# Kernel tuning notes

Measured on AMD Instinct MI355X. Metric: run time of the kernel, lower is better.

## Reference

```python
import jax, jax.numpy as jnp
import numpy as np

VOCAB = 50000
EMB = 300      # embedding_dim
VDIM = 16      # value_dim
QDIM = 200     # query_dim
NHEAD = 16     # head_num
HIDDEN = VDIM * NHEAD  # 256


def setup_inputs() -> dict:
    key = jax.random.key(0)
    ks = jax.random.split(key, 9)
    news_batch = jax.random.randint(ks[0], (32, 50, 20), 0, VOCAB)  # [B, his, L]
    emb_table = jax.random.normal(ks[1], (VOCAB, EMB), dtype=jnp.float32)
    queryWeight = jax.random.normal(ks[2], (NHEAD, EMB, EMB), dtype=jnp.float32) * 0.05
    queryBias = jax.random.normal(ks[3], (NHEAD, 1, EMB), dtype=jnp.float32) * 0.05
    valueWeight = jax.random.normal(ks[4], (NHEAD, EMB, VDIM), dtype=jnp.float32) * 0.05
    valueBias = jax.random.normal(ks[5], (NHEAD, 1, VDIM), dtype=jnp.float32) * 0.05
    keyW = jax.random.normal(ks[6], (QDIM, HIDDEN), dtype=jnp.float32) * 0.05  # nn.Linear weight [out,in]
    keyB = jax.random.normal(ks[7], (QDIM,), dtype=jnp.float32) * 0.05
    query = jax.random.normal(ks[8], (1, QDIM), dtype=jnp.float32)
    return {"news_batch": news_batch, "emb_table": emb_table,
            "queryWeight": queryWeight, "queryBias": queryBias,
            "valueWeight": valueWeight, "valueBias": valueBias,
            "keyW": keyW, "keyB": keyB, "query": query}


def reference(news_batch, emb_table, queryWeight, queryBias, valueWeight, valueBias, keyW, keyB, query):
    # Dropout in eval mode -> identity.
    x = emb_table[news_batch]                                   # [B,S,L,E]
    B, S, L, E = x.shape
    # per-head query projection: mha_key.matmul(queryWeight) + queryBias
    q = jnp.einsum('bsle,nef->bsnlf', x, queryWeight) + queryBias  # [B,S,N,L,E]
    # ScaledDpAttention(q, key=x, value=x), scale by sqrt(query last dim) = sqrt(E)
    scores = jnp.einsum('bsnlf,bsmf->bsnlm', q, x) / jnp.sqrt(jnp.float32(E))
    attn = jax.nn.softmax(scores, axis=-1)
    ctx = jnp.einsum('bsnlm,bsme->bsnle', attn, x)               # [B,S,N,L,E]
    v = jnp.einsum('bsnle,nev->bsnlv', ctx, valueWeight) + valueBias  # [B,S,N,L,V]
    # transpose(-2,-3) then merge heads -> [B,S,L,N*V]
    mha_embedding = jnp.swapaxes(v, -2, -3).reshape(B, S, L, HIDDEN)
    # additive attention pooling
    add_key = jnp.tanh(mha_embedding @ keyW.T + keyB)            # [B,S,L,QDIM]
    s2 = jnp.einsum('qd,bsld->bsql', query, add_key) / jnp.sqrt(jnp.float32(QDIM))
    a2 = jax.nn.softmax(s2, axis=-1)                             # [B,S,1,L]
    news_repr = jnp.einsum('bsql,bslh->bsqh', a2, mha_embedding)[:, :, 0, :]  # [B,S,H]
    news_embedding = mha_embedding.reshape(B, S, L, 1, HIDDEN)   # level=1
    return news_embedding, news_repr
```

## Files before the change

kernel.cpp:

```cpp
#include <hip/hip_runtime.h>
#include <math.h>

#define NBS 1600
#define LL 20
#define EE 300
#define NH 16
#define VD 16
#define HID 256
#define QD 200

typedef short bf16x8 __attribute__((ext_vector_type(8)));
typedef float f32x4 __attribute__((ext_vector_type(4)));

__device__ __forceinline__ short f2b(float f) {
    union { float f; unsigned u; } c; c.f = f;
    unsigned r = (c.u + 0x7FFFu + ((c.u >> 16) & 1u)) >> 16;
    return (short)r;
}

__device__ __forceinline__ float b2f(short s) {
    union { unsigned u; float f; } c; c.u = ((unsigned)(unsigned short)s) << 16;
    return c.f;
}

__device__ __forceinline__ float ftanh(float a) {
    a = fminf(fmaxf(a, -15.f), 15.f);
    float t = __expf(2.f * a);
    return (t - 1.f) / (t + 1.f);
}

__device__ __forceinline__ void gload16(const short* g, short* l) {
    __builtin_amdgcn_global_load_lds(
        (const __attribute__((address_space(1))) unsigned int*)g,
        (__attribute__((address_space(3))) unsigned int*)l, 16, 0, 0);
}


__global__ void build_xb_lin(const int* __restrict__ news, const float* __restrict__ emb,
                             short* __restrict__ Xb) {
    int idx = blockIdx.x * 256 + threadIdx.x;
    if (idx >= 32000 * 80) return;
    int i = idx / 80, e4 = (idx % 80) * 4;
    short4 o;
    if (e4 < 300) {
        const float4 v = *reinterpret_cast<const float4*>(emb + (size_t)news[i] * EE + e4);
        o.x = f2b(v.x); o.y = f2b(v.y); o.z = f2b(v.z); o.w = f2b(v.w);
    } else if (e4 == 300) {
        o.x = (short)0x3F80; o.y = 0; o.z = 0; o.w = 0;
    } else {
        o.x = o.y = o.z = o.w = 0;
    }
    *reinterpret_cast<short4*>(Xb + (size_t)i * 320 + e4) = o;
}

__global__ __launch_bounds__(1024) void build_wqt_lin(
    const float* __restrict__ qW, const float* __restrict__ qB, short* __restrict__ WqT)
{
    __shared__ float t[32][33];
    const int n = blockIdx.z;
    const int e0 = blockIdx.x * 32, f0 = blockIdx.y * 32;
    const int tx = threadIdx.x, ty = threadIdx.y;
    const int e = e0 + ty, f = f0 + tx;
    t[ty][tx] = (e < EE && f < EE) ? qW[((size_t)n * EE + e) * EE + f] : 0.f;
    __syncthreads();
    const int fo = f0 + ty, eo = e0 + tx;
    float val;
    if (fo >= EE)      val = 0.f;
    else if (eo < EE)  val = t[tx][ty];
    else if (eo == EE) val = qB[n * EE + fo];
    else               val = 0.f;
    WqT[((size_t)n * 320 + fo) * 320 + eo] = f2b(val);
}

__global__ void build_wvt(const float* __restrict__ vW, const float* __restrict__ vB,
                          short* __restrict__ WvT) {
    int idx = blockIdx.x * 256 + threadIdx.x;
    if (idx >= 256 * 320) return;
    int c = idx / 320, e = idx % 320;
    int n = c >> 4, vd = c & 15;
    float val = (e < EE) ? vW[((size_t)n * EE + e) * VD + vd]
                         : (e == EE ? vB[n * VD + vd] : 0.f);
    WvT[idx] = f2b(val);
}

__global__ void conv_kw(const float* __restrict__ keyW, short* __restrict__ kwb) {
    int idx = blockIdx.x * 256 + threadIdx.x;
    if (idx >= 256 * 256) return;
    int d = idx >> 8;
    kwb[idx] = (d < QD) ? f2b(keyW[idx]) : (short)0;
}

__global__ __launch_bounds__(256) void gemm_xv(
    const short* __restrict__ Xb, const short* __restrict__ WvT, short* __restrict__ xv)
{
    const int nt0 = blockIdx.x * 128;
    const size_t mt0 = (size_t)blockIdx.y * 128;
    const int tid = threadIdx.x, wave = tid >> 6, lane = tid & 63;
    const int lr = lane & 15, lg = lane >> 4;
    const int wm = wave & 1, wn = wave >> 1;

    __shared__ short As[128][68];
    __shared__ short Bs[128][68];
    f32x4 acc[4][4] = {};

    for (int ks = 0; ks < 5; ++ks) {
        __syncthreads();
        for (int u = 0; u < 4; ++u) {
            int idx = u * 256 + tid;
            int rr = idx >> 3, c8 = idx & 7;
            *reinterpret_cast<bf16x8*>(&As[rr][c8 * 8]) =
                *reinterpret_cast<const bf16x8*>(Xb + (mt0 + rr) * 320 + ks * 64 + c8 * 8);
            *reinterpret_cast<bf16x8*>(&Bs[rr][c8 * 8]) =
                *reinterpret_cast<const bf16x8*>(WvT + (size_t)(nt0 + rr) * 320 + ks * 64 + c8 * 8);
        }
        __syncthreads();
        #pragma unroll
        for (int kk = 0; kk < 2; ++kk) {
            bf16x8 af[4], bfv[4];
            #pragma unroll
            for (int f = 0; f < 4; ++f)
                af[f] = *reinterpret_cast<const bf16x8*>(&As[wm * 64 + f * 16 + lr][kk * 32 + lg * 8]);
            #pragma unroll
            for (int f = 0; f < 4; ++f)
                bfv[f] = *reinterpret_cast<const bf16x8*>(&Bs[wn * 64 + f * 16 + lr][kk * 32 + lg * 8]);
            #pragma unroll
            for (int i = 0; i < 4; ++i)
                #pragma unroll
                for (int j = 0; j < 4; ++j)
                    acc[i][j] = __builtin_amdgcn_mfma_f32_16x16x32_bf16(af[i], bfv[j], acc[i][j], 0, 0, 0);
        }
    }
    #pragma unroll
    for (int i = 0; i < 4; ++i)
        #pragma unroll
        for (int j = 0; j < 4; ++j)
            #pragma unroll
            for (int r = 0; r < 4; ++r)
                xv[(mt0 + wm * 64 + i * 16 + lg * 4 + r) * 256 + nt0 + wn * 64 + j * 16 + lr]
                    = f2b(acc[i][j][r]);
}

__global__ __launch_bounds__(256, 2) void qsv(
    const short* __restrict__ Xb,
    const short* __restrict__ WqT,
    const short* __restrict__ xv,
    float*       __restrict__ out1,
    short*       __restrict__ mhb)
{
    const int g = blockIdx.x;
    const int n = blockIdx.y;
    const int tid = threadIdx.x, wave = tid >> 6, lane = tid & 63;
    const int lr = lane & 15, lg = lane >> 4;
    const size_t row0 = (size_t)g * 80;

    __shared__ short lds[25920];

    const short* gp[13];
    #pragma unroll
    for (int k = 0; k < 13; ++k) {
        const int s = k * 256 + tid;
        if (s < 640) {
            const int row = s >> 3, p = s & 7;
            gp[k] = Xb + (row0 + row) * 320 + (p ^ (row & 7)) * 8;
        } else if (s < 3200) {
            const int s2 = s - 640;
            const int row = s2 >> 3, p = s2 & 7;
            gp[k] = WqT + (size_t)(n * 320 + row) * 320 + (p ^ (row & 7)) * 8;
        } else {
            gp[k] = Xb;
        }
    }

    const int b = wave;
    bf16x8 bv;
    #pragma unroll
    for (int j = 0; j < 8; ++j) {
        int m = lg * 8 + j; if (m > 19) m = 19;
        bv[j] = xv[(row0 + b * 20 + m) * 256 + n * 16 + lr];
    }

    const int sw = (lr & 7);

    f32x4 acc[5][5] = {};
    for (int ks = 0; ks < 5; ++ks) {
        __syncthreads();
        const int ko = ks * 64;
        #pragma unroll
        for (int k = 0; k < 12; ++k)
            gload16(gp[k] + ko, lds + (size_t)(k * 256 + tid) * 8);
        if (tid < 128)
            gload16(gp[12] + ko, lds + (size_t)(3072 + tid) * 8);
        __syncthreads();
        #pragma unroll
        for (int sub = 0; sub < 2; ++sub) {
            bf16x8 af[5], bfr[5];
            #pragma unroll
            for (int i = 0; i < 5; ++i)
                af[i] = *reinterpret_cast<const bf16x8*>(
                    lds + (i * 16 + lr) * 64 + ((sub * 4 + lg) ^ sw) * 8);
            #pragma unroll
            for (int j = 0; j < 5; ++j)
                bfr[j] = *reinterpret_cast<const bf16x8*>(
                    lds + 5120 + (wave * 80 + j * 16 + lr) * 64 + ((sub * 4 + lg) ^ sw) * 8);
            #pragma unroll
            for (int i = 0; i < 5; ++i)
                #pragma unroll
                for (int j = 0; j < 5; ++j)
                    acc[i][j] = __builtin_amdgcn_mfma_f32_16x16x32_bf16(af[i], bfr[j], acc[i][j], 0, 0, 0);
        }
    }
    __syncthreads();

    #pragma unroll
    for (int i = 0; i < 5; ++i)
        #pragma unroll
        for (int j = 0; j < 5; ++j)
            #pragma unroll
            for (int r = 0; r < 4; ++r)
                lds[(i * 16 + lg * 4 + r) * 324 + wave * 80 + j * 16 + lr] = f2b(acc[i][j][r]);

    const int rA0 = b * 20 + lr;
    int rA1 = b * 20 + 16 + lr; if (rA1 > 79) rA1 = 79;
    bf16x8 xpre0[10], xpre1[10];
    #pragma unroll
    for (int ks = 0; ks < 10; ++ks) {
        xpre0[ks] = *reinterpret_cast<const bf16x8*>(Xb + (row0 + rA0) * 320 + ks * 32 + lg * 8);
        xpre1[ks] = *reinterpret_cast<const bf16x8*>(Xb + (row0 + rA1) * 320 + ks * 32 + lg * 8);
    }
    __syncthreads();

    float w0[2][4], w1[2][4];
    {
        f32x4 s[2][2] = {};
        #pragma unroll
        for (int ks = 0; ks < 10; ++ks) {
            const int kc = ks * 32 + lg * 8;
            bf16x8 a0 = *reinterpret_cast<const bf16x8*>(lds + rA0 * 324 + kc);
            bf16x8 a1 = *reinterpret_cast<const bf16x8*>(lds + rA1 * 324 + kc);
            s[0][0] = __builtin_amdgcn_mfma_f32_16x16x32_bf16(a0, xpre0[ks], s[0][0], 0, 0, 0);
            s[0][1] = __builtin_amdgcn_mfma_f32_16x16x32_bf16(a0, xpre1[ks], s[0][1], 0, 0, 0);
            s[1][0] = __builtin_amdgcn_mfma_f32_16x16x32_bf16(a1, xpre0[ks], s[1][0], 0, 0, 0);
            s[1][1] = __builtin_amdgcn_mfma_f32_16x16x32_bf16(a1, xpre1[ks], s[1][1], 0, 0, 0);
        }

        const float scl = 0.057735026918962584f;
        #pragma unroll
        for (int mts = 0; mts < 2; ++mts) {
            #pragma unroll
            for (int r = 0; r < 4; ++r) {
                float v0 = s[mts][0][r] * scl;
                float v1 = s[mts][1][r] * scl;
                float mx = (lr < 4) ? fmaxf(v0, v1) : v0;
                mx = fmaxf(mx, __shfl_xor(mx, 1));
                mx = fmaxf(mx, __shfl_xor(mx, 2));
                mx = fmaxf(mx, __shfl_xor(mx, 4));
                mx = fmaxf(mx, __shfl_xor(mx, 8));
                float e0 = __expf(v0 - mx);
                float e1 = (lr < 4) ? __expf(v1 - mx) : 0.f;
                float sm = e0 + e1;
                sm += __shfl_xor(sm, 1);
                sm += __shfl_xor(sm, 2);
                sm += __shfl_xor(sm, 4);
                sm += __shfl_xor(sm, 8);
                const float inv = 1.f / sm;
                w0[mts][r] = e0 * inv;
                w1[mts][r] = e1 * inv;
            }
        }
    }

    short* atw = lds + b * 6480;
    {
        int* az = reinterpret_cast<int*>(atw);
        #pragma unroll
        for (int i = 0; i < 9; ++i) {
            const int ix = lane + i * 64;
            if (ix < 544) az[ix] = 0;
        }
    }
    #pragma unroll
    for (int mts = 0; mts < 2; ++mts)
        #pragma unroll
        for (int r = 0; r < 4; ++r) {
            const int row = mts * 16 + lg * 4 + r;
            if (row < LL) {
                atw[row * 34 + lr]      = f2b(w0[mts][r]);
                atw[row * 34 + 16 + lr] = f2b(w1[mts][r]);
            }
        }

    bf16x8 va0 = *reinterpret_cast<const bf16x8*>(atw + lr * 34 + lg * 8);
    bf16x8 va1 = *reinterpret_cast<const bf16x8*>(atw + (16 + lr) * 34 + lg * 8);
    f32x4 z = {0.f, 0.f, 0.f, 0.f};
    f32x4 v0 = __builtin_amdgcn_mfma_f32_16x16x32_bf16(va0, bv, z, 0, 0, 0);
    f32x4 v1 = __builtin_amdgcn_mfma_f32_16x16x32_bf16(va1, bv, z, 0, 0, 0);
    #pragma unroll
    for (int r = 0; r < 4; ++r) {
        const int rowl = lg * 4 + r;
        const size_t o0 = (row0 + b * 20 + rowl) * 256 + n * 16 + lr;
        out1[o0] = v0[r];
        mhb[o0] = f2b(v0[r]);
        const int rowl1 = 16 + lg * 4 + r;
        if (rowl1 < LL) {
            const size_t o1 = (row0 + b * 20 + rowl1) * 256 + n * 16 + lr;
            out1[o1] = v1[r];
            mhb[o1] = f2b(v1[r]);
        }
    }
}

__global__ __launch_bounds__(256, 4) void gemm_ak(
    const short* __restrict__ mhb,
    const short* __restrict__ kwb,
    short*       __restrict__ ak)
{
    const int nt0 = blockIdx.x * 128;
    const int mt0 = blockIdx.y * 128;
    const int tid = threadIdx.x, wave = tid >> 6, lane = tid & 63;
    const int lr = lane & 15, lg = lane >> 4;
    const int wm = wave & 1, wn = wave >> 1;

    __shared__ short sAB[8192];

    const int rA = tid >> 2, c = tid & 3;
    const short* aS0 = mhb + (size_t)(mt0 + rA) * 256 + c * 8;
    const short* aS1 = aS0 + (size_t)64 * 256;
    const short* bS0 = kwb + (size_t)(nt0 + rA) * 256 + c * 8;
    const short* bS1 = bS0 + (size_t)64 * 256;
    short* d0 = sAB + tid * 8;
    short* d1 = sAB + (tid + 256) * 8;
    short* d2 = sAB + (tid + 512) * 8;
    short* d3 = sAB + (tid + 768) * 8;

    f32x4 acc[4][4] = {};
    for (int ks = 0; ks < 8; ++ks) {
        __syncthreads();
        const int ko = ks * 32;
        gload16(aS0 + ko, d0);
        gload16(aS1 + ko, d1);
        gload16(bS0 + ko, d2);
        gload16(bS1 + ko, d3);
        __syncthreads();
        bf16x8 af[4], bfr[4];
        #pragma unroll
        for (int i = 0; i < 4; ++i)
            af[i] = *reinterpret_cast<const bf16x8*>(sAB + (wm * 64 + i * 16 + lr) * 32 + lg * 8);
        #pragma unroll
        for (int j = 0; j < 4; ++j)
            bfr[j] = *reinterpret_cast<const bf16x8*>(sAB + 4096 + (wn * 64 + j * 16 + lr) * 32 + lg * 8);
        #pragma unroll
        for (int i = 0; i < 4; ++i)
            #pragma unroll
            for (int j = 0; j < 4; ++j)
                acc[i][j] = __builtin_amdgcn_mfma_f32_16x16x32_bf16(af[i], bfr[j], acc[i][j], 0, 0, 0);
    }

    #pragma unroll
    for (int i = 0; i < 4; ++i)
        #pragma unroll
        for (int j = 0; j < 4; ++j)
            #pragma unroll
            for (int r = 0; r < 4; ++r)
                ak[(size_t)(mt0 + wm * 64 + i * 16 + lg * 4 + r) * 256
                   + nt0 + wn * 64 + j * 16 + lr] = f2b(acc[i][j][r]);
}

__global__ __launch_bounds__(256) void pool_light(
    const short* __restrict__ ak,
    const float* __restrict__ out1,
    const float* __restrict__ keyB,
    const float* __restrict__ query,
    float*       __restrict__ out2)
{
    const int bs = blockIdx.x;
    const int tid = threadIdx.x, wave = tid >> 6, lane = tid & 63;

    __shared__ float s2[LL];

    #pragma unroll
    for (int li = 0; li < 5; ++li) {
        const int l = wave * 5 + li;
        const short* ar = ak + ((size_t)bs * 20 + l) * 256;
        float acc = 0.f;
        #pragma unroll
        for (int it = 0; it < 4; ++it) {
            const int d = lane + it * 64;
            if (d < QD) {
                const float t = ftanh(b2f(ar[d]) + keyB[d]);
                acc = fmaf(query[d], t, acc);
            }
        }
        acc += __shfl_xor(acc, 32);
        acc += __shfl_xor(acc, 16);
        acc += __shfl_xor(acc, 8);
        acc += __shfl_xor(acc, 4);
        acc += __shfl_xor(acc, 2);
        acc += __shfl_xor(acc, 1);
        if (lane == 0) s2[l] = acc * 0.07071067811865475f;
    }
    __syncthreads();

    if (tid == 0) {
        float mx = -1e30f;
        #pragma unroll
        for (int l = 0; l < LL; ++l) mx = fmaxf(mx, s2[l]);
        float e[LL], sum = 0.f;
        #pragma unroll
        for (int l = 0; l < LL; ++l) { e[l] = __expf(s2[l] - mx); sum += e[l]; }
        const float inv = 1.f / sum;
        #pragma unroll
        for (int l = 0; l < LL; ++l) s2[l] = e[l] * inv;
    }
    __syncthreads();

    float o = 0.f;
    #pragma unroll
    for (int l = 0; l < LL; ++l)
        o = fmaf(s2[l], out1[((size_t)bs * 20 + l) * 256 + tid], o);
    out2[(size_t)bs * 256 + tid] = o;
}


#define XP 330
#define TP 42
#define AP 34

__global__ __launch_bounds__(1024) void transpose_qw(
    const float* __restrict__ qW, short* __restrict__ wqt)
{
    __shared__ float t[32][33];
    const int n = blockIdx.z;
    const int e0 = blockIdx.x * 32, f0 = blockIdx.y * 32;
    const int tx = threadIdx.x, ty = threadIdx.y;
    const int e = e0 + ty, f = f0 + tx;
    t[ty][tx] = (e < EE && f < EE) ? qW[(size_t)n * EE * EE + e * EE + f] : 0.f;
    __syncthreads();
    const int fo = f0 + ty, eo = e0 + tx;
    if (fo < 304)
        wqt[(size_t)n * 304 * 320 + fo * 320 + eo] = f2b(t[tx][ty]);
}

__global__ void conv_vw(const float* __restrict__ vW, short* __restrict__ wvt) {
    int idx = blockIdx.x * 256 + threadIdx.x;
    if (idx >= NH * VD * 320) return;
    int e = idx % 320;
    int v = (idx / 320) % VD;
    int n = idx / (320 * VD);
    wvt[idx] = (e < EE) ? f2b(vW[(size_t)n * EE * VD + e * VD + v]) : (short)0;
}

__global__ __launch_bounds__(512) void nrms_attn_mfma(
    const int*   __restrict__ news,
    const float* __restrict__ emb,
    const short* __restrict__ wqt,
    const float* __restrict__ qB,
    const short* __restrict__ wvt,
    const float* __restrict__ vB,
    float*       __restrict__ out1)
{
    const int bs   = blockIdx.x;
    const int tid  = threadIdx.x;
    const int wave = tid >> 6;
    const int lane = tid & 63;
    const int lr   = lane & 15;
    const int lg   = lane >> 4;

    __shared__ short xs[32][XP];
    __shared__ short xT[320][TP];
    __shared__ short qs[32][XP];
    __shared__ float sc[32][33];
    __shared__ short at[32][AP];

    {
        int* z = (int*)&xs[0][0];
        for (int i = tid; i < 32 * XP / 2; i += 512) z[i] = 0;
        z = (int*)&qs[0][0];
        for (int i = tid; i < 32 * XP / 2; i += 512) z[i] = 0;
        z = (int*)&xT[0][0];
        for (int i = tid; i < 320 * TP / 2; i += 512) z[i] = 0;
    }
    __syncthreads();

    for (int idx = tid; idx < LL * 75; idx += 512) {
        const int l = idx / 75, e4 = (idx % 75) * 4;
        const int row = news[bs * LL + l];
        const float4 v = *reinterpret_cast<const float4*>(emb + (size_t)row * EE + e4);
        const short b0 = f2b(v.x), b1 = f2b(v.y), b2 = f2b(v.z), b3 = f2b(v.w);
        xs[l][e4] = b0; xs[l][e4 + 1] = b1; xs[l][e4 + 2] = b2; xs[l][e4 + 3] = b3;
        xT[e4][l] = b0; xT[e4 + 1][l] = b1; xT[e4 + 2][l] = b2; xT[e4 + 3][l] = b3;
    }
    __syncthreads();

    for (int n = 0; n < NH; ++n) {
        const short* wq = wqt + (size_t)n * 304 * 320;

        for (int p = wave; p < 19; p += 8) {
            f32x4 acc0 = {0.f, 0.f, 0.f, 0.f};
            f32x4 acc1 = {0.f, 0.f, 0.f, 0.f};
            const short* a0p = &xs[lr][lg * 8];
            const short* a1p = &xs[16 + lr][lg * 8];
            const short* bp  = wq + (p * 16 + lr) * 320 + lg * 8;
            #pragma unroll
            for (int k = 0; k < 10; ++k) {
                bf16x8 b  = *reinterpret_cast<const bf16x8*>(bp + k * 32);
                bf16x8 a0 = *reinterpret_cast<const bf16x8*>(a0p + k * 32);
                bf16x8 a1 = *reinterpret_cast<const bf16x8*>(a1p + k * 32);
                acc0 = __builtin_amdgcn_mfma_f32_16x16x32_bf16(a0, b, acc0, 0, 0, 0);
                acc1 = __builtin_amdgcn_mfma_f32_16x16x32_bf16(a1, b, acc1, 0, 0, 0);
            }
            const int col = p * 16 + lr;
            const float bias = (col < EE) ? qB[n * EE + col] : 0.f;
            #pragma unroll
            for (int r = 0; r < 4; ++r) {
                qs[lg * 4 + r][col]      = f2b(acc0[r] + bias);
                qs[16 + lg * 4 + r][col] = f2b(acc1[r] + bias);
            }
        }
        __syncthreads();

        if (wave < 4) {
            const int mt = wave & 1, nt = wave >> 1;
            f32x4 acc = {0.f, 0.f, 0.f, 0.f};
            const short* ap = &qs[mt * 16 + lr][lg * 8];
            const short* bp = &xs[nt * 16 + lr][lg * 8];
            #pragma unroll
            for (int k = 0; k < 10; ++k) {
                bf16x8 a = *reinterpret_cast<const bf16x8*>(ap + k * 32);
                bf16x8 b = *reinterpret_cast<const bf16x8*>(bp + k * 32);
                acc = __builtin_amdgcn_mfma_f32_16x16x32_bf16(a, b, acc, 0, 0, 0);
            }
            #pragma unroll
            for (int r = 0; r < 4; ++r)
                sc[mt * 16 + lg * 4 + r][nt * 16 + lr] = acc[r] * 0.057735026918962584f;
        }
        __syncthreads();

        if (tid < LL) {
            float mx = -1e30f;
            #pragma unroll
            for (int m = 0; m < LL; ++m) mx = fmaxf(mx, sc[tid][m]);
            float ev[LL], sum = 0.f;
            #pragma unroll
            for (int m = 0; m < LL; ++m) { ev[m] = __expf(sc[tid][m] - mx); sum += ev[m]; }
            const float inv = 1.f / sum;
            #pragma unroll
            for (int m = 0; m < LL; ++m) at[tid][m] = f2b(ev[m] * inv);
            #pragma unroll
            for (int m = LL; m < 32; ++m) at[tid][m] = 0;
        } else if (tid < 32) {
            int* zr = (int*)&at[tid][0];
            #pragma unroll
            for (int m = 0; m < 16; ++m) zr[m] = 0;
        }
        __syncthreads();

        for (int p = wave; p < 19; p += 8) {
            bf16x8 b  = *reinterpret_cast<const bf16x8*>(&xT[p * 16 + lr][lg * 8]);
            bf16x8 a0 = *reinterpret_cast<const bf16x8*>(&at[lr][lg * 8]);
            bf16x8 a1 = *reinterpret_cast<const bf16x8*>(&at[16 + lr][lg * 8]);
            f32x4 z = {0.f, 0.f, 0.f, 0.f};
            f32x4 c0 = __builtin_amdgcn_mfma_f32_16x16x32_bf16(a0, b, z, 0, 0, 0);
            f32x4 c1 = __builtin_amdgcn_mfma_f32_16x16x32_bf16(a1, b, z, 0, 0, 0);
            const int col = p * 16 + lr;
            #pragma unroll
            for (int r = 0; r < 4; ++r) {
                qs[lg * 4 + r][col]      = f2b(c0[r]);
                qs[16 + lg * 4 + r][col] = f2b(c1[r]);
            }
        }
        __syncthreads();

        if (wave < 2) {
            const int mt = wave;
            f32x4 acc = {0.f, 0.f, 0.f, 0.f};
            const short* ap = &qs[mt * 16 + lr][lg * 8];
            const short* bp = wvt + (size_t)n * VD * 320 + lr * 320 + lg * 8;
            #pragma unroll
            for (int k = 0; k < 10; ++k) {
                bf16x8 a = *reinterpret_cast<const bf16x8*>(ap + k * 32);
                bf16x8 b = *reinterpret_cast<const bf16x8*>(bp + k * 32);
                acc = __builtin_amdgcn_mfma_f32_16x16x32_bf16(a, b, acc, 0, 0, 0);
            }
            #pragma unroll
            for (int r = 0; r < 4; ++r) {
                const int row = mt * 16 + lg * 4 + r;
                if (row < LL)
                    out1[((size_t)bs * LL + row) * HID + n * VD + lr] = acc[r] + vB[n * VD + lr];
            }
        }
        __syncthreads();
    }
}

__global__ __launch_bounds__(256) void nrms_pool_mfma(
    const float* __restrict__ out1,
    const short* __restrict__ kwb,
    const float* __restrict__ keyB,
    const float* __restrict__ query,
    float*       __restrict__ out2)
{
    const int bs   = blockIdx.x;
    const int tid  = threadIdx.x;
    const int wave = tid >> 6;
    const int lane = tid & 63;
    const int lr   = lane & 15;
    const int lg   = lane >> 4;

    __shared__ float mh[LL][257];
    __shared__ short mhbl[32][264];
    __shared__ float s2p[32];

    for (int i = tid; i < 12 * 128; i += 256) {
        const int r = 20 + i / 128, c = (i % 128) * 2;
        *reinterpret_cast<int*>(&mhbl[r][c]) = 0;
    }
    if (tid < 32) s2p[tid] = 0.f;

    for (int idx = tid; idx < LL * 64; idx += 256) {
        const int l = idx >> 6, h4 = (idx & 63) * 4;
        const float4 v = *reinterpret_cast<const float4*>(out1 + ((size_t)bs * LL + l) * HID + h4);
        mh[l][h4] = v.x; mh[l][h4 + 1] = v.y; mh[l][h4 + 2] = v.z; mh[l][h4 + 3] = v.w;
        mhbl[l][h4] = f2b(v.x); mhbl[l][h4 + 1] = f2b(v.y);
        mhbl[l][h4 + 2] = f2b(v.z); mhbl[l][h4 + 3] = f2b(v.w);
    }
    __syncthreads();

    for (int t = wave; t < 26; t += 4) {
        const int mt = t & 1, nt = t >> 1;
        f32x4 acc = {0.f, 0.f, 0.f, 0.f};
        const short* ap = &mhbl[mt * 16 + lr][lg * 8];
        const short* bp = kwb + (nt * 16 + lr) * 256 + lg * 8;
        #pragma unroll
        for (int k = 0; k < 8; ++k) {
            bf16x8 a = *reinterpret_cast<const bf16x8*>(ap + k * 32);
            bf16x8 b = *reinterpret_cast<const bf16x8*>(bp + k * 32);
            acc = __builtin_amdgcn_mfma_f32_16x16x32_bf16(a, b, acc, 0, 0, 0);
        }
        const int d = nt * 16 + lr;
        const float qd = (d < QD) ? query[d] : 0.f;
        const float kb = (d < QD) ? keyB[d] : 0.f;
        float vals[4];
        #pragma unroll
        for (int r = 0; r < 4; ++r) vals[r] = qd * ftanh(acc[r] + kb);
        #pragma unroll
        for (int off = 1; off < 16; off <<= 1) {
            #pragma unroll
            for (int r = 0; r < 4; ++r) vals[r] += __shfl_xor(vals[r], off);
        }
        if (lr == 0) {
            #pragma unroll
            for (int r = 0; r < 4; ++r)
                atomicAdd(&s2p[mt * 16 + lg * 4 + r], vals[r]);
        }
    }
    __syncthreads();

    if (tid == 0) {
        float mx = -1e30f;
        #pragma unroll
        for (int l = 0; l < LL; ++l) mx = fmaxf(mx, s2p[l] * 0.07071067811865475f);
        float sum = 0.f;
        float e[LL];
        #pragma unroll
        for (int l = 0; l < LL; ++l) { e[l] = __expf(s2p[l] * 0.07071067811865475f - mx); sum += e[l]; }
        const float inv = 1.f / sum;
        #pragma unroll
        for (int l = 0; l < LL; ++l) s2p[l] = e[l] * inv;
    }
    __syncthreads();

    {
        const int h = tid;
        float acc = 0.f;
        #pragma unroll
        for (int l = 0; l < LL; ++l) acc = fmaf(s2p[l], mh[l][h], acc);
        out2[(size_t)bs * HID + h] = acc;
    }
}


extern "C" void kernel_launch(void* const* d_in, const int* in_sizes, int n_in,
                              void* d_out, int out_size, void* d_ws, size_t ws_size,
                              hipStream_t stream) {
    const int*   news  = (const int*)d_in[0];
    const float* emb   = (const float*)d_in[1];
    const float* qW    = (const float*)d_in[2];
    const float* qB    = (const float*)d_in[3];
    const float* vW    = (const float*)d_in[4];
    const float* vB    = (const float*)d_in[5];
    const float* keyW  = (const float*)d_in[6];
    const float* keyB  = (const float*)d_in[7];
    const float* query = (const float*)d_in[8];

    float* out1 = (float*)d_out;
    float* out2 = out1 + 8192000;

    const size_t BASE_SH = 10240000ull + 1638400 + 81920 + 8192000
                         + 65536 + 8192000 + 8192000;
    const size_t BASE_B  = BASE_SH * 2;

    if (ws_size >= BASE_B) {
        short* Xb   = (short*)d_ws;
        short* WqT  = Xb + 10240000;
        short* WvT  = WqT + 1638400;
        short* xv   = WvT + 81920;
        short* kwb2 = xv + 8192000;
        short* mhb  = kwb2 + 65536;
        short* ak   = mhb + 8192000;

        hipLaunchKernelGGL(build_xb_lin, dim3(10000), dim3(256), 0, stream, news, emb, Xb);
        hipLaunchKernelGGL(build_wqt_lin, dim3(10, 10, 16), dim3(32, 32), 0, stream, qW, qB, WqT);
        hipLaunchKernelGGL(build_wvt, dim3(320), dim3(256), 0, stream, vW, vB, WvT);
        hipLaunchKernelGGL(conv_kw, dim3(256), dim3(256), 0, stream, keyW, kwb2);
        hipLaunchKernelGGL(gemm_xv, dim3(2, 250), dim3(256), 0, stream, Xb, WvT, xv);
        hipLaunchKernelGGL(qsv, dim3(400, 16), dim3(256), 0, stream,
                           Xb, WqT, xv, out1, mhb);
        hipLaunchKernelGGL(gemm_ak, dim3(2, 250), dim3(256), 0, stream, mhb, kwb2, ak);
        hipLaunchKernelGGL(pool_light, dim3(NBS), dim3(256), 0, stream,
                           ak, out1, keyB, query, out2);
    } else {
        short* wqt  = (short*)d_ws;
        short* wvt  = wqt + (size_t)NH * 304 * 320;
        short* kwb2 = wvt + (size_t)NH * VD * 320;

        hipLaunchKernelGGL(transpose_qw, dim3(10, 10, 16), dim3(32, 32), 0, stream, qW, wqt);
        hipLaunchKernelGGL(conv_vw, dim3(320), dim3(256), 0, stream, vW, wvt);
        hipLaunchKernelGGL(conv_kw, dim3(256), dim3(256), 0, stream, keyW, kwb2);
        hipLaunchKernelGGL(nrms_attn_mfma, dim3(NBS), dim3(512), 0, stream,
                           news, emb, wqt, qB, wvt, vB, out1);
        hipLaunchKernelGGL(nrms_pool_mfma, dim3(NBS), dim3(256), 0, stream,
                           out1, kwb2, keyB, query, out2);
    }
}
```

Before: 253.0 us.

## Fuse tanh-query scoring into key GEMM epilogue and merge prep kernels

The additive-attention key GEMM now applies bias, tanh and the query dot product in its epilogue, reducing each row to two per-N-tile partial scores. This removes the bf16 ak intermediate write and its re-read in the pooling kernel. The pooling kernel then only sums the partials before the softmax and weighted sum. The three small conversion kernels (embedding gather, value weight, key weight) are merged into one launch to cut launch overhead. The epilogue gains extra transcendental work and shuffles, and the score no longer passes through a bf16 rounding of the pre-activation.

```diff
diff --git a/kernel.cpp b/kernel.cpp
--- a/kernel.cpp
+++ b/kernel.cpp
@@ -36,21 +36,40 @@
 }
 
 
-__global__ void build_xb_lin(const int* __restrict__ news, const float* __restrict__ emb,
-                             short* __restrict__ Xb) {
+__global__ void build_all(const int* __restrict__ news, const float* __restrict__ emb,
+                          const float* __restrict__ vW, const float* __restrict__ vB,
+                          const float* __restrict__ keyW,
+                          short* __restrict__ Xb, short* __restrict__ WvT,
+                          short* __restrict__ kwb) {
     int idx = blockIdx.x * 256 + threadIdx.x;
-    if (idx >= 32000 * 80) return;
-    int i = idx / 80, e4 = (idx % 80) * 4;
-    short4 o;
-    if (e4 < 300) {
-        const float4 v = *reinterpret_cast<const float4*>(emb + (size_t)news[i] * EE + e4);
-        o.x = f2b(v.x); o.y = f2b(v.y); o.z = f2b(v.z); o.w = f2b(v.w);
-    } else if (e4 == 300) {
-        o.x = (short)0x3F80; o.y = 0; o.z = 0; o.w = 0;
-    } else {
-        o.x = o.y = o.z = o.w = 0;
-    }
-    *reinterpret_cast<short4*>(Xb + (size_t)i * 320 + e4) = o;
+    if (idx < 2560000) {
+        int i = idx / 80, e4 = (idx % 80) * 4;
+        short4 o;
+        if (e4 < 300) {
+            const float4 v = *reinterpret_cast<const float4*>(emb + (size_t)news[i] * EE + e4);
+            o.x = f2b(v.x); o.y = f2b(v.y); o.z = f2b(v.z); o.w = f2b(v.w);
+        } else if (e4 == 300) {
+            o.x = (short)0x3F80; o.y = 0; o.z = 0; o.w = 0;
+        } else {
+            o.x = o.y = o.z = o.w = 0;
+        }
+        *reinterpret_cast<short4*>(Xb + (size_t)i * 320 + e4) = o;
+        return;
+    }
+    idx -= 2560000;
+    if (idx < 81920) {
+        int c = idx / 320, e = idx % 320;
+        int n = c >> 4, vd = c & 15;
+        float val = (e < EE) ? vW[((size_t)n * EE + e) * VD + vd]
+                             : (e == EE ? vB[n * VD + vd] : 0.f);
+        WvT[idx] = f2b(val);
+        return;
+    }
+    idx -= 81920;
+    if (idx < 65536) {
+        int d = idx >> 8;
+        kwb[idx] = (d < QD) ? f2b(keyW[idx]) : (short)0;
+    }
 }
 
 __global__ __launch_bounds__(1024) void build_wqt_lin(
@@ -70,24 +89,6 @@
     else if (eo == EE) val = qB[n * EE + fo];
     else               val = 0.f;
     WqT[((size_t)n * 320 + fo) * 320 + eo] = f2b(val);
-}
-
-__global__ void build_wvt(const float* __restrict__ vW, const float* __restrict__ vB,
-                          short* __restrict__ WvT) {
-    int idx = blockIdx.x * 256 + threadIdx.x;
-    if (idx >= 256 * 320) return;
-    int c = idx / 320, e = idx % 320;
-    int n = c >> 4, vd = c & 15;
-    float val = (e < EE) ? vW[((size_t)n * EE + e) * VD + vd]
-                         : (e == EE ? vB[n * VD + vd] : 0.f);
-    WvT[idx] = f2b(val);
-}
-
-__global__ void conv_kw(const float* __restrict__ keyW, short* __restrict__ kwb) {
-    int idx = blockIdx.x * 256 + threadIdx.x;
-    if (idx >= 256 * 256) return;
-    int d = idx >> 8;
-    kwb[idx] = (d < QD) ? f2b(keyW[idx]) : (short)0;
 }
 
 __global__ __launch_bounds__(256) void gemm_xv(
@@ -309,10 +310,12 @@
     }
 }
 
-__global__ __launch_bounds__(256, 4) void gemm_ak(
+__global__ __launch_bounds__(256, 4) void gemm_ak2(
     const short* __restrict__ mhb,
     const short* __restrict__ kwb,
-    short*       __restrict__ ak)
+    const float* __restrict__ keyB,
+    const float* __restrict__ query,
+    float*       __restrict__ s2p)
 {
     const int nt0 = blockIdx.x * 128;
     const int mt0 = blockIdx.y * 128;
@@ -321,6 +324,7 @@
     const int wm = wave & 1, wn = wave >> 1;
 
     __shared__ short sAB[8192];
+    __shared__ float part[128][2];
 
     const int rA = tid >> 2, c = tid & 3;
     const short* aS0 = mhb + (size_t)(mt0 + rA) * 256 + c * 8;
@@ -358,45 +362,40 @@
     #pragma unroll
     for (int i = 0; i < 4; ++i)
         #pragma unroll
-        for (int j = 0; j < 4; ++j)
-            #pragma unroll
-            for (int r = 0; r < 4; ++r)
-                ak[(size_t)(mt0 + wm * 64 + i * 16 + lg * 4 + r) * 256
-                   + nt0 + wn * 64 + j * 16 + lr] = f2b(acc[i][j][r]);
-}
-
-__global__ __launch_bounds__(256) void pool_light(
-    const short* __restrict__ ak,
+        for (int r = 0; r < 4; ++r) {
+            float vsum = 0.f;
+            #pragma unroll
+            for (int j = 0; j < 4; ++j) {
+                const int d = nt0 + wn * 64 + j * 16 + lr;
+                if (d < QD)
+                    vsum = fmaf(query[d], ftanh(acc[i][j][r] + keyB[d]), vsum);
+            }
+            vsum += __shfl_xor(vsum, 1);
+            vsum += __shfl_xor(vsum, 2);
+            vsum += __shfl_xor(vsum, 4);
+            vsum += __shfl_xor(vsum, 8);
+            if (lr == 0)
+                part[wm * 64 + i * 16 + lg * 4 + r][wn] = vsum;
+        }
+    __syncthreads();
+
+    if (tid < 128)
+        s2p[(size_t)(mt0 + tid) * 2 + blockIdx.x] = part[tid][0] + part[tid][1];
+}
+
+__global__ __launch_bounds__(256) void pool_final(
+    const float* __restrict__ s2p,
     const float* __restrict__ out1,
-    const float* __restrict__ keyB,
-    const float* __restrict__ query,
     float*       __restrict__ out2)
 {
     const int bs = blockIdx.x;
-    const int tid = threadIdx.x, wave = tid >> 6, lane = tid & 63;
+    const int tid = threadIdx.x;
 
     __shared__ float s2[LL];
 
-    #pragma unroll
-    for (int li = 0; li < 5; ++li) {
-        const int l = wave * 5 + li;
-        const short* ar = ak + ((size_t)bs * 20 + l) * 256;
-        float acc = 0.f;
-        #pragma unroll
-        for (int it = 0; it < 4; ++it) {
-            const int d = lane + it * 64;
-            if (d < QD) {
-                const float t = ftanh(b2f(ar[d]) + keyB[d]);
-                acc = fmaf(query[d], t, acc);
-            }
-        }
-        acc += __shfl_xor(acc, 32);
-        acc += __shfl_xor(acc, 16);
-        acc += __shfl_xor(acc, 8);
-        acc += __shfl_xor(acc, 4);
-        acc += __shfl_xor(acc, 2);
-        acc += __shfl_xor(acc, 1);
-        if (lane == 0) s2[l] = acc * 0.07071067811865475f;
+    if (tid < LL) {
+        const size_t row = (size_t)bs * 20 + tid;
+        s2[tid] = (s2p[row * 2] + s2p[row * 2 + 1]) * 0.07071067811865475f;
     }
     __syncthreads();
 
@@ -447,6 +446,13 @@
     int v = (idx / 320) % VD;
     int n = idx / (320 * VD);
     wvt[idx] = (e < EE) ? f2b(vW[(size_t)n * EE * VD + e * VD + v]) : (short)0;
+}
+
+__global__ void conv_kw_fb(const float* __restrict__ keyW, short* __restrict__ kwb) {
+    int idx = blockIdx.x * 256 + threadIdx.x;
+    if (idx >= 256 * 256) return;
+    int d = idx >> 8;
+    kwb[idx] = (d < QD) ? f2b(keyW[idx]) : (short)0;
 }
 
 __global__ __launch_bounds__(512) void nrms_attn_mfma(
@@ -696,7 +702,7 @@
     float* out2 = out1 + 8192000;
 
     const size_t BASE_SH = 10240000ull + 1638400 + 81920 + 8192000
-                         + 65536 + 8192000 + 8192000;
+                         + 65536 + 8192000 + 128000;
     const size_t BASE_B  = BASE_SH * 2;
 
     if (ws_size >= BASE_B) {
@@ -706,18 +712,17 @@
         short* xv   = WvT + 81920;
         short* kwb2 = xv + 8192000;
         short* mhb  = kwb2 + 65536;
-        short* ak   = mhb + 8192000;
-
-        hipLaunchKernelGGL(build_xb_lin, dim3(10000), dim3(256), 0, stream, news, emb, Xb);
+        float* s2p  = (float*)(mhb + 8192000);
+
+        hipLaunchKernelGGL(build_all, dim3(10577), dim3(256), 0, stream,
+                           news, emb, vW, vB, keyW, Xb, WvT, kwb2);
         hipLaunchKernelGGL(build_wqt_lin, dim3(10, 10, 16), dim3(32, 32), 0, stream, qW, qB, WqT);
-        hipLaunchKernelGGL(build_wvt, dim3(320), dim3(256), 0, stream, vW, vB, WvT);
-        hipLaunchKernelGGL(conv_kw, dim3(256), dim3(256), 0, stream, keyW, kwb2);
         hipLaunchKernelGGL(gemm_xv, dim3(2, 250), dim3(256), 0, stream, Xb, WvT, xv);
         hipLaunchKernelGGL(qsv, dim3(400, 16), dim3(256), 0, stream,
                            Xb, WqT, xv, out1, mhb);
-        hipLaunchKernelGGL(gemm_ak, dim3(2, 250), dim3(256), 0, stream, mhb, kwb2, ak);
-        hipLaunchKernelGGL(pool_light, dim3(NBS), dim3(256), 0, stream,
-                           ak, out1, keyB, query, out2);
+        hipLaunchKernelGGL(gemm_ak2, dim3(2, 250), dim3(256), 0, stream,
+                           mhb, kwb2, keyB, query, s2p);
+        hipLaunchKernelGGL(pool_final, dim3(NBS), dim3(256), 0, stream, s2p, out1, out2);
     } else {
         short* wqt  = (short*)d_ws;
         short* wvt  = wqt + (size_t)NH * 304 * 320;
@@ -725,7 +730,7 @@
 
         hipLaunchKernelGGL(transpose_qw, dim3(10, 10, 16), dim3(32, 32), 0, stream, qW, wqt);
         hipLaunchKernelGGL(conv_vw, dim3(320), dim3(256), 0, stream, vW, wvt);
-        hipLaunchKernelGGL(conv_kw, dim3(256), dim3(256), 0, stream, keyW, kwb2);
+        hipLaunchKernelGGL(conv_kw_fb, dim3(256), dim3(256), 0, stream, keyW, kwb2);
         hipLaunchKernelGGL(nrms_attn_mfma, dim3(NBS), dim3(512), 0, stream,
                            news, emb, wqt, qB, wvt, vB, out1);
         hipLaunchKernelGGL(nrms_pool_mfma, dim3(NBS), dim3(256), 0, stream,
```

Measured after the change: 249.3 us, median of 2. About the same (-1.5%).
